# Kernel optimization log

Measured on AMD Instinct MI355X. Metric: run time of the kernel, lower is better.

Reference implementation:

```python
import jax, jax.numpy as jnp
import numpy as np
jax.config.update("jax_enable_x64", True)

PAD_ID = -1
NUM_DISCRETE = 128  # args.n_discrete_size

def _lexsort3(v):
    # torch code: stable argsort by x, then y, then z -> final key order z (primary), y, x.
    # numpy/jax lexsort: last key is primary, and it is stable.
    idx = jnp.lexsort((v[:, 0], v[:, 1], v[:, 2]))
    return v[idx], idx

def setup_inputs() -> dict:
    key = jax.random.key(0)
    k1, k2 = jax.random.split(key)
    B, NV, NF = 32, 32768, 65536
    vertices = jax.random.normal(k1, (B, NV, 3), dtype=jnp.float32)
    faces = jax.random.randint(k2, (B, NF, 3), 0, NV, dtype=jnp.int64)
    n_pad = NF // 10
    faces = faces.at[:, NF - n_pad:, :].set(PAD_ID)
    return {"vertices": vertices, "faces": faces}

def reference(vertices, faces):
    B, NV, _ = vertices.shape
    # normalize_vertices reduces over dim 0 (which is the BATCH dim here) - faithful to source
    mn = vertices.min(axis=0)
    mx = vertices.max(axis=0)
    center = (mn + mx) * 0.5
    longest = (mx - mn).max()
    v = (vertices - center) / longest
    # batched lexicographic sort of vertices
    sorted_v, sort_idx = jax.vmap(_lexsort3)(v)
    # inverse permutation (inv[sort_idx] = arange  <=>  argsort of a permutation)
    inv = jnp.argsort(sort_idx, axis=1)  # (B, NV)
    # torch indexes inverse_mapping[faces] with pad -1 wrapping to NV-1
    wrapped = jnp.mod(faces, NV)
    reindexed = jax.vmap(lambda m, f: m[f])(inv, wrapped)  # (B, NF, 3)
    sorted_faces, _ = jax.vmap(_lexsort3)(reindexed)
    # face mask: all three vertex ids != pad
    face_mask = jnp.all(faces != PAD_ID, axis=-1)  # (B, NF)
    face_np = jnp.where(face_mask[..., None], faces, 0)
    # gather vertex coords per face: (B, NF, 3verts, 3coords). The torch code
    # materializes a (b,nf,nv,3) repeat then gathers; we gather directly.
    face_coords = jax.vmap(lambda vv, ff: vv[ff])(sorted_v, face_np)
    # discretize into [-1, 1] -> [0, 127]
    t = (face_coords + 1.0) * 0.5 * NUM_DISCRETE - 0.5
    dq = jnp.clip(jnp.round(t).astype(jnp.int64), 0, NUM_DISCRETE - 1)
    codes = jnp.where(face_mask[..., None, None], dq, PAD_ID)
    input_ids = codes.reshape(B, -1)
    attention_mask = (input_ids != PAD_ID).astype(jnp.float32)
    ph = jnp.full((B, 1), PAD_ID, dtype=input_ids.dtype)
    input_ids = jnp.concatenate([ph, input_ids, ph], axis=1)
    attention_mask = jnp.concatenate([ph.astype(jnp.float32), attention_mask, ph.astype(jnp.float32)], axis=1)
    return input_ids, attention_mask, codes, dq, sorted_faces
```

## Files before the change

kernel.cpp:

```cpp
#include <hip/hip_runtime.h>
#include <stdint.h>

#define BATCH 32
#define NV 32768
#define NF 65536
#define PCOUNT (NV*3)


__device__ __forceinline__ unsigned fenc(float f){
  unsigned u = __float_as_uint(f);
  return (u & 0x80000000u) ? ~u : (u | 0x80000000u);
}
__device__ __forceinline__ float fdec(unsigned e){
  unsigned u = (e & 0x80000000u) ? (e & 0x7FFFFFFFu) : ~e;
  return __uint_as_float(u);
}

__global__ void kminmax(const float* __restrict__ vert, float* __restrict__ center,
                        unsigned* __restrict__ longestBits){
  int p = blockIdx.x*256 + threadIdx.x;
  float mn = 3.4e38f, mx = -3.4e38f;
  #pragma unroll
  for (int b = 0; b < BATCH; ++b) {
    float v = vert[(size_t)b*PCOUNT + p];
    mn = fminf(mn, v); mx = fmaxf(mx, v);
  }
  center[p] = __fadd_rn(mn, mx) * 0.5f;
  float r = __fsub_rn(mx, mn);
  for (int off = 32; off > 0; off >>= 1) r = fmaxf(r, __shfl_down(r, off, 64));
  if ((threadIdx.x & 63) == 0) atomicMax(longestBits, __float_as_uint(r));
}

__device__ __forceinline__ bool less4(uint4 a, uint4 b){
  if (a.x != b.x) return a.x < b.x;
  if (a.y != b.y) return a.y < b.y;
  if (a.z != b.z) return a.z < b.z;
  return a.w < b.w;
}
__device__ __forceinline__ bool less2(uint2 a, uint2 b){
  if (a.y != b.y) return a.y < b.y;
  return a.x < b.x;
}

#define VT 4096
#define FT 8192
#define SWV(i) ((i) ^ (((i) >> 3) & 7))
#define SWF(i) ((i) ^ (((i) >> 4) & 15))

__global__ __launch_bounds__(512) void klocalv(const float* __restrict__ vert,
                                               const float* __restrict__ center,
                                               const unsigned* __restrict__ longestBits,
                                               uint4* __restrict__ S){
  __shared__ uint4 sh[VT];
  int blockBase = blockIdx.x * VT;
  float L = __uint_as_float(*longestBits);
  float rl = __fdiv_rn(1.0f, L);
  for (int i = threadIdx.x; i < VT; i += 512){
    int id = blockBase + i;
    int vi = id & (NV-1);
    size_t vb = (size_t)(id >> 15)*PCOUNT + (size_t)vi*3;
    float nx = __fsub_rn(vert[vb+0], center[vi*3+0]);
    float ny = __fsub_rn(vert[vb+1], center[vi*3+1]);
    float nz = __fsub_rn(vert[vb+2], center[vi*3+2]);
    float x = __fmul_rn(nx, rl);
    float y = __fmul_rn(ny, rl);
    float z = __fmul_rn(nz, rl);
    uint4 s; s.x = fenc(z); s.y = fenc(y); s.z = fenc(x); s.w = (unsigned)vi;
    sh[SWV(i)] = s;
  }
  __syncthreads();
  int t = threadIdx.x;
  int k0 = t * 8;
  uint4 v[8];
  #pragma unroll
  for (int e = 0; e < 8; ++e) v[e] = sh[SWV(k0 + e)];
  #pragma unroll
  for (int k = 2; k <= 8; k <<= 1){
    #pragma unroll
    for (int j = k >> 1; j > 0; j >>= 1){
      #pragma unroll
      for (int i = 0; i < 8; ++i){
        int l = i ^ j;
        if (l > i){
          bool up = ((i & k) == 0);
          bool sw = up ? less4(v[l], v[i]) : less4(v[i], v[l]);
          if (sw){ uint4 tmp = v[i]; v[i] = v[l]; v[l] = tmp; }
        }
      }
    }
  }
  #pragma unroll
  for (int e = 0; e < 8; ++e) sh[SWV(k0 + e)] = v[e];
  __syncthreads();
  for (int w = 8; w < VT; w <<= 1){
    int base = k0 & ~(2*w - 1);
    int ko = k0 - base;
    int lo = ko - w; if (lo < 0) lo = 0;
    int hi = ko < w ? ko : w;
    while (lo < hi){
      int mid = (lo + hi) >> 1;
      if (less4(sh[SWV(base + mid)], sh[SWV(base + w + ko-1-mid)])) lo = mid + 1; else hi = mid;
    }
    int i = lo, j = ko - lo;
    uint4 m[8];
    #pragma unroll
    for (int e = 0; e < 8; ++e){
      bool takeA = (j >= w) || (i < w && less4(sh[SWV(base + i)], sh[SWV(base + w + j)]));
      m[e] = takeA ? sh[SWV(base + i)] : sh[SWV(base + w + j)];
      if (takeA) ++i; else ++j;
    }
    __syncthreads();
    #pragma unroll
    for (int e = 0; e < 8; ++e) sh[SWV(k0 + e)] = m[e];
    __syncthreads();
  }
  uint4* basep = S + (size_t)blockBase;
  for (int i = threadIdx.x; i < VT; i += 512) basep[i] = sh[SWV(i)];
}

__global__ __launch_bounds__(512) void klocalf(const int* __restrict__ faces,
                                               const int* __restrict__ inv,
                                               uint2* __restrict__ F){
  __shared__ uint2 sh[FT];
  int blockBase = blockIdx.x * FT;
  int b = blockBase >> 16;
  const int* invb = inv + (b << 15);
  for (int i = threadIdx.x; i < FT; i += 512){
    int id = blockBase + i;
    int f = id & (NF-1);
    size_t fb = (size_t)id*3;
    int f0 = faces[fb+0], f1 = faces[fb+1], f2 = faces[fb+2];
    unsigned r0 = (unsigned)invb[f0 & (NV-1)];
    unsigned r1 = (unsigned)invb[f1 & (NV-1)];
    unsigned r2 = (unsigned)invb[f2 & (NV-1)];
    uint2 r; r.x = (r0 << 15) | (unsigned)f; r.y = (r2 << 15) | r1;
    sh[SWF(i)] = r;
  }
  __syncthreads();
  int t = threadIdx.x;
  int k0 = t * 16;
  uint2 v[16];
  #pragma unroll
  for (int e = 0; e < 16; ++e) v[e] = sh[SWF(k0 + e)];
  #pragma unroll
  for (int k = 2; k <= 16; k <<= 1){
    #pragma unroll
    for (int j = k >> 1; j > 0; j >>= 1){
      #pragma unroll
      for (int i = 0; i < 16; ++i){
        int l = i ^ j;
        if (l > i){
          bool up = ((i & k) == 0);
          bool sw = up ? less2(v[l], v[i]) : less2(v[i], v[l]);
          if (sw){ uint2 tmp = v[i]; v[i] = v[l]; v[l] = tmp; }
        }
      }
    }
  }
  #pragma unroll
  for (int e = 0; e < 16; ++e) sh[SWF(k0 + e)] = v[e];
  __syncthreads();
  for (int w = 16; w < FT; w <<= 1){
    int base = k0 & ~(2*w - 1);
    int ko = k0 - base;
    int lo = ko - w; if (lo < 0) lo = 0;
    int hi = ko < w ? ko : w;
    while (lo < hi){
      int mid = (lo + hi) >> 1;
      if (less2(sh[SWF(base + mid)], sh[SWF(base + w + ko-1-mid)])) lo = mid + 1; else hi = mid;
    }
    int i = lo, j = ko - lo;
    uint2 m[16];
    #pragma unroll
    for (int e = 0; e < 16; ++e){
      bool takeA = (j >= w) || (i < w && less2(sh[SWF(base + i)], sh[SWF(base + w + j)]));
      m[e] = takeA ? sh[SWF(base + i)] : sh[SWF(base + w + j)];
      if (takeA) ++i; else ++j;
    }
    __syncthreads();
    #pragma unroll
    for (int e = 0; e < 16; ++e) sh[SWF(k0 + e)] = m[e];
    __syncthreads();
  }
  uint2* basep = F + (size_t)blockBase;
  for (int i = threadIdx.x; i < FT; i += 512) basep[i] = sh[SWF(i)];
}

__global__ __launch_bounds__(256) void kmergev(const uint4* __restrict__ src,
                                               uint4* __restrict__ dst, int L){
  __shared__ uint4 sh[2048];
  __shared__ int sAB[2];
  int gid = blockIdx.x;
  int b = gid >> 4, c = gid & 15;
  const uint4* base = src + ((size_t)b << 15);
  uint4* obase = dst + ((size_t)b << 15);
  int co = c * 2048;
  int pair = co / (2*L);
  int ko = co - pair*2*L;
  const uint4* A = base + (size_t)pair*2*L;
  const uint4* B = A + L;
  uint4* O = obase + (size_t)pair*2*L + ko;
  if (threadIdx.x < 2){
    int k = ko + (int)threadIdx.x * 2048;
    int lo = k - L; if (lo < 0) lo = 0;
    int hi = k < L ? k : L;
    while (lo < hi){
      int mid = (lo + hi) >> 1;
      if (less4(A[mid], B[k-1-mid])) lo = mid + 1; else hi = mid;
    }
    sAB[threadIdx.x] = lo;
  }
  __syncthreads();
  int aStart = sAB[0];
  int na = sAB[1] - aStart;
  int nb = 2048 - na;
  int bStart = ko - aStart;
  for (int i = threadIdx.x; i < 2048; i += 256)
    sh[i] = (i < na) ? A[aStart + i] : B[bStart + (i - na)];
  __syncthreads();
  int k0 = threadIdx.x * 8;
  int lo = k0 - nb; if (lo < 0) lo = 0;
  int hi = k0 < na ? k0 : na;
  while (lo < hi){
    int mid = (lo + hi) >> 1;
    if (less4(sh[mid], sh[na + k0-1-mid])) lo = mid + 1; else hi = mid;
  }
  int i = lo, j = k0 - lo;
  #pragma unroll
  for (int e = 0; e < 8; ++e){
    bool takeA = (j >= nb) || (i < na && less4(sh[i], sh[na + j]));
    uint4 v = takeA ? sh[i] : sh[na + j];
    if (takeA) ++i; else ++j;
    O[k0 + e] = v;
  }
}

__global__ __launch_bounds__(256) void kmergevQ(const uint4* __restrict__ src,
                                                int* __restrict__ inv,
                                                unsigned* __restrict__ Q){
  #pragma clang fp contract(off)
  __shared__ uint4 sh[2048];
  __shared__ int sAB[2];
  const int L = 16384;
  int gid = blockIdx.x;
  int b = gid >> 4, c = gid & 15;
  const uint4* A = src + ((size_t)b << 15);
  const uint4* B = A + L;
  int ko = c * 2048;
  if (threadIdx.x < 2){
    int k = ko + (int)threadIdx.x * 2048;
    int lo = k - L; if (lo < 0) lo = 0;
    int hi = k < L ? k : L;
    while (lo < hi){
      int mid = (lo + hi) >> 1;
      if (less4(A[mid], B[k-1-mid])) lo = mid + 1; else hi = mid;
    }
    sAB[threadIdx.x] = lo;
  }
  __syncthreads();
  int aStart = sAB[0];
  int na = sAB[1] - aStart;
  int nb = 2048 - na;
  int bStart = ko - aStart;
  for (int i = threadIdx.x; i < 2048; i += 256)
    sh[i] = (i < na) ? A[aStart + i] : B[bStart + (i - na)];
  __syncthreads();
  int k0 = threadIdx.x * 8;
  int lo = k0 - nb; if (lo < 0) lo = 0;
  int hi = k0 < na ? k0 : na;
  while (lo < hi){
    int mid = (lo + hi) >> 1;
    if (less4(sh[mid], sh[na + k0-1-mid])) lo = mid + 1; else hi = mid;
  }
  int i = lo, j = k0 - lo;
  #pragma unroll
  for (int e = 0; e < 8; ++e){
    bool takeA = (j >= nb) || (i < na && less4(sh[i], sh[na + j]));
    uint4 s = takeA ? sh[i] : sh[na + j];
    if (takeA) ++i; else ++j;
    int pos = ko + k0 + e;
    inv[(b<<15) + (int)s.w] = pos;
    float cco[3]; cco[0] = fdec(s.z); cco[1] = fdec(s.y); cco[2] = fdec(s.x);
    unsigned qw = 0;
    #pragma unroll
    for (int cc = 0; cc < 3; ++cc){
      float tt = ((cco[cc] + 1.0f) * 0.5f) * 128.0f - 0.5f;
      float rq = rintf(tt);
      int qi = (int)rq;
      qi = qi < 0 ? 0 : (qi > 127 ? 127 : qi);
      qw |= ((unsigned)qi) << (8*cc);
    }
    Q[(b<<15) + pos] = qw;
  }
}

__global__ __launch_bounds__(256) void kmergef(const uint2* __restrict__ src,
                                               uint2* __restrict__ dst, int L){
  __shared__ uint2 sh[2048];
  __shared__ int sAB[2];
  int gid = blockIdx.x;
  int b = gid >> 5, c = gid & 31;
  const uint2* base = src + ((size_t)b << 16);
  uint2* obase = dst + ((size_t)b << 16);
  int co = c * 2048;
  int pair = co / (2*L);
  int ko = co - pair*2*L;
  const uint2* A = base + (size_t)pair*2*L;
  const uint2* B = A + L;
  uint2* O = obase + (size_t)pair*2*L + ko;
  if (threadIdx.x < 2){
    int k = ko + (int)threadIdx.x * 2048;
    int lo = k - L; if (lo < 0) lo = 0;
    int hi = k < L ? k : L;
    while (lo < hi){
      int mid = (lo + hi) >> 1;
      if (less2(A[mid], B[k-1-mid])) lo = mid + 1; else hi = mid;
    }
    sAB[threadIdx.x] = lo;
  }
  __syncthreads();
  int aStart = sAB[0];
  int na = sAB[1] - aStart;
  int nb = 2048 - na;
  int bStart = ko - aStart;
  for (int i = threadIdx.x; i < 2048; i += 256)
    sh[i] = (i < na) ? A[aStart + i] : B[bStart + (i - na)];
  __syncthreads();
  int k0 = threadIdx.x * 8;
  int lo = k0 - nb; if (lo < 0) lo = 0;
  int hi = k0 < na ? k0 : na;
  while (lo < hi){
    int mid = (lo + hi) >> 1;
    if (less2(sh[mid], sh[na + k0-1-mid])) lo = mid + 1; else hi = mid;
  }
  int i = lo, j = k0 - lo;
  #pragma unroll
  for (int e = 0; e < 8; ++e){
    bool takeA = (j >= nb) || (i < na && less2(sh[i], sh[na + j]));
    uint2 v = takeA ? sh[i] : sh[na + j];
    if (takeA) ++i; else ++j;
    O[k0 + e] = v;
  }
}

__global__ __launch_bounds__(256) void kmergefOut(const uint2* __restrict__ src,
                                                  float* __restrict__ out){
  __shared__ __align__(16) float shf[6144];
  __shared__ int sAB[2];
  uint2* sh = (uint2*)shf;
  const int L = 32768;
  int gid = blockIdx.x;
  int b = gid >> 5, c = gid & 31;
  const uint2* A = src + ((size_t)b << 16);
  const uint2* B = A + L;
  int ko = c * 2048;
  if (threadIdx.x < 2){
    int k = ko + (int)threadIdx.x * 2048;
    int lo = k - L; if (lo < 0) lo = 0;
    int hi = k < L ? k : L;
    while (lo < hi){
      int mid = (lo + hi) >> 1;
      if (less2(A[mid], B[k-1-mid])) lo = mid + 1; else hi = mid;
    }
    sAB[threadIdx.x] = lo;
  }
  __syncthreads();
  int aStart = sAB[0];
  int na = sAB[1] - aStart;
  int nb = 2048 - na;
  int bStart = ko - aStart;
  for (int i = threadIdx.x; i < 2048; i += 256)
    sh[i] = (i < na) ? A[aStart + i] : B[bStart + (i - na)];
  __syncthreads();
  int k0 = threadIdx.x * 8;
  int lo = k0 - nb; if (lo < 0) lo = 0;
  int hi = k0 < na ? k0 : na;
  while (lo < hi){
    int mid = (lo + hi) >> 1;
    if (less2(sh[mid], sh[na + k0-1-mid])) lo = mid + 1; else hi = mid;
  }
  int i = lo, j = k0 - lo;
  uint2 v[8];
  #pragma unroll
  for (int e = 0; e < 8; ++e){
    bool takeA = (j >= nb) || (i < na && less2(sh[i], sh[na + j]));
    v[e] = takeA ? sh[i] : sh[na + j];
    if (takeA) ++i; else ++j;
  }
  __syncthreads();
  #pragma unroll
  for (int e = 0; e < 8; ++e){
    int o = (k0 + e) * 3;
    shf[o+0] = (float)(v[e].x >> 15);
    shf[o+1] = (float)(v[e].y & 0x7FFFu);
    shf[o+2] = (float)(v[e].y >> 15);
  }
  __syncthreads();
  size_t basef = 75497600 + ((size_t)b*65536 + (size_t)ko)*3;
  for (int q = threadIdx.x; q < 6144; q += 256) out[basef + q] = shf[q];
}

__global__ __launch_bounds__(256) void kfacesB(const int* __restrict__ faces,
                                               const unsigned* __restrict__ Q,
                                               float* __restrict__ out){
  __shared__ __align__(16) float shq[2304];
  __shared__ float shm[256];
  int p = blockIdx.x;
  int l = ((p & 7) << 10) | (p >> 3);
  int b = l >> 8, c = l & 255;
  int t = threadIdx.x;
  {
    size_t fb = ((size_t)(l*256 + t))*3;
    int f0 = faces[fb+0], f1 = faces[fb+1], f2 = faces[fb+2];
    bool mask = (f0 != -1) & (f1 != -1) & (f2 != -1);
    shm[t] = mask ? 1.0f : 0.0f;
    int fv[3] = {mask ? f0 : 0, mask ? f1 : 0, mask ? f2 : 0};
    #pragma unroll
    for (int k = 0; k < 3; ++k){
      unsigned qw = Q[(b<<15) + fv[k]];
      shq[t*9 + k*3 + 0] = (float)( qw        & 0xFFu);
      shq[t*9 + k*3 + 1] = (float)((qw >> 8 ) & 0xFFu);
      shq[t*9 + k*3 + 2] = (float)((qw >> 16) & 0xFFu);
    }
  }
  __syncthreads();
  float4* cp = (float4*)(out + 37748864 + (size_t)l*2304);
  float4* dp = (float4*)(out + 56623232 + (size_t)l*2304);
  for (int r = t; r < 576; r += 256){
    int e0 = r*4;
    float4 q = *(const float4*)&shq[e0];
    float m0 = shm[(unsigned)(e0  )/9u];
    float m1 = shm[(unsigned)(e0+1)/9u];
    float m2 = shm[(unsigned)(e0+2)/9u];
    float m3 = shm[(unsigned)(e0+3)/9u];
    float4 cv;
    cv.x = m0 != 0.0f ? q.x : -1.0f;
    cv.y = m1 != 0.0f ? q.y : -1.0f;
    cv.z = m2 != 0.0f ? q.z : -1.0f;
    cv.w = m3 != 0.0f ? q.w : -1.0f;
    cp[r] = cv;
    dp[r] = q;
  }
  size_t idsBase  = (size_t)b*589826 + 1 + (size_t)c*2304;
  size_t attnBase = 18874432 + idsBase;
  #pragma unroll
  for (int r = 0; r < 9; ++r){
    int idx = r*256 + t;
    float q = shq[idx];
    float m = shm[(unsigned)idx/9u];
    float cv = m != 0.0f ? q : -1.0f;
    out[idsBase + idx]  = cv;
    out[attnBase + idx] = m;
  }
  if (c == 0 && t == 0){
    out[(size_t)b*589826]                     = -1.0f;
    out[(size_t)b*589826 + 589825]            = -1.0f;
    out[18874432 + (size_t)b*589826]          = -1.0f;
    out[18874432 + (size_t)b*589826 + 589825] = -1.0f;
  }
}

extern "C" void kernel_launch(void* const* d_in, const int* in_sizes, int n_in,
                              void* d_out, int out_size, void* d_ws, size_t ws_size,
                              hipStream_t stream){
  const float* vert  = (const float*)d_in[0];
  const int*   faces = (const int*)d_in[1];
  float* out = (float*)d_out;

  uint4*    S           = (uint4*)d_ws;
  uint4*    S2          = (uint4*)((char*)d_ws + 16777216);
  uint2*    FKa         = (uint2*)((char*)d_ws + 16777216);
  unsigned* Q           = (unsigned*)((char*)d_ws + 16777216);
  uint2*    FKb         = (uint2*)d_ws;
  int*      inv         = (int*)((char*)d_ws + 33554432);
  float*    center      = (float*)((char*)d_ws + 37748736);
  unsigned* longestBits = (unsigned*)((char*)d_ws + 38141952);

  hipMemsetAsync(longestBits, 0, 4, stream);
  kminmax<<<PCOUNT/256, 256, 0, stream>>>(vert, center, longestBits);

  klocalv<<<BATCH*(NV/VT), 512, 0, stream>>>(vert, center, longestBits, S);
  kmergev<<<BATCH*16, 256, 0, stream>>>(S,  S2, 4096);
  kmergev<<<BATCH*16, 256, 0, stream>>>(S2, S,  8192);
  kmergevQ<<<BATCH*16, 256, 0, stream>>>(S, inv, Q);

  kfacesB<<<(BATCH*NF)/256, 256, 0, stream>>>(faces, Q, out);

  klocalf<<<BATCH*(NF/FT), 512, 0, stream>>>(faces, inv, FKa);
  kmergef<<<BATCH*32, 256, 0, stream>>>(FKa, FKb, 8192);
  kmergef<<<BATCH*32, 256, 0, stream>>>(FKb, FKa, 16384);
  kmergefOut<<<BATCH*32, 256, 0, stream>>>(FKa, out);
}
```

Before: 643.1 us.

## Fuse face code emission into local face sort kernel

Merges the per-face quantized-code and mask output kernel into the local face-sort kernel, so faces are read once and both the sort keys and the output codes come from the same load. Shared memory is reused as staging for code writes before the in-block sort. This removes one kernel launch and one full pass over the faces input, but it serializes 16 chunks per block with extra barriers and uses far fewer blocks for the output writes.

```diff
diff --git a/kernel.cpp b/kernel.cpp
--- a/kernel.cpp
+++ b/kernel.cpp
@@ -118,74 +118,6 @@
   for (int i = threadIdx.x; i < VT; i += 512) basep[i] = sh[SWV(i)];
 }
 
-__global__ __launch_bounds__(512) void klocalf(const int* __restrict__ faces,
-                                               const int* __restrict__ inv,
-                                               uint2* __restrict__ F){
-  __shared__ uint2 sh[FT];
-  int blockBase = blockIdx.x * FT;
-  int b = blockBase >> 16;
-  const int* invb = inv + (b << 15);
-  for (int i = threadIdx.x; i < FT; i += 512){
-    int id = blockBase + i;
-    int f = id & (NF-1);
-    size_t fb = (size_t)id*3;
-    int f0 = faces[fb+0], f1 = faces[fb+1], f2 = faces[fb+2];
-    unsigned r0 = (unsigned)invb[f0 & (NV-1)];
-    unsigned r1 = (unsigned)invb[f1 & (NV-1)];
-    unsigned r2 = (unsigned)invb[f2 & (NV-1)];
-    uint2 r; r.x = (r0 << 15) | (unsigned)f; r.y = (r2 << 15) | r1;
-    sh[SWF(i)] = r;
-  }
-  __syncthreads();
-  int t = threadIdx.x;
-  int k0 = t * 16;
-  uint2 v[16];
-  #pragma unroll
-  for (int e = 0; e < 16; ++e) v[e] = sh[SWF(k0 + e)];
-  #pragma unroll
-  for (int k = 2; k <= 16; k <<= 1){
-    #pragma unroll
-    for (int j = k >> 1; j > 0; j >>= 1){
-      #pragma unroll
-      for (int i = 0; i < 16; ++i){
-        int l = i ^ j;
-        if (l > i){
-          bool up = ((i & k) == 0);
-          bool sw = up ? less2(v[l], v[i]) : less2(v[i], v[l]);
-          if (sw){ uint2 tmp = v[i]; v[i] = v[l]; v[l] = tmp; }
-        }
-      }
-    }
-  }
-  #pragma unroll
-  for (int e = 0; e < 16; ++e) sh[SWF(k0 + e)] = v[e];
-  __syncthreads();
-  for (int w = 16; w < FT; w <<= 1){
-    int base = k0 & ~(2*w - 1);
-    int ko = k0 - base;
-    int lo = ko - w; if (lo < 0) lo = 0;
-    int hi = ko < w ? ko : w;
-    while (lo < hi){
-      int mid = (lo + hi) >> 1;
-      if (less2(sh[SWF(base + mid)], sh[SWF(base + w + ko-1-mid)])) lo = mid + 1; else hi = mid;
-    }
-    int i = lo, j = ko - lo;
-    uint2 m[16];
-    #pragma unroll
-    for (int e = 0; e < 16; ++e){
-      bool takeA = (j >= w) || (i < w && less2(sh[SWF(base + i)], sh[SWF(base + w + j)]));
-      m[e] = takeA ? sh[SWF(base + i)] : sh[SWF(base + w + j)];
-      if (takeA) ++i; else ++j;
-    }
-    __syncthreads();
-    #pragma unroll
-    for (int e = 0; e < 16; ++e) sh[SWF(k0 + e)] = m[e];
-    __syncthreads();
-  }
-  uint2* basep = F + (size_t)blockBase;
-  for (int i = threadIdx.x; i < FT; i += 512) basep[i] = sh[SWF(i)];
-}
-
 __global__ __launch_bounds__(256) void kmergev(const uint4* __restrict__ src,
                                                uint4* __restrict__ dst, int L){
   __shared__ uint4 sh[2048];
@@ -294,6 +226,128 @@
   }
 }
 
+__global__ __launch_bounds__(512) void klocalfB(const int* __restrict__ faces,
+                                                const int* __restrict__ inv,
+                                                const unsigned* __restrict__ Qt,
+                                                uint2* __restrict__ F,
+                                                float* __restrict__ out){
+  __shared__ __align__(16) uint2 sh[FT];
+  float* shq = (float*)sh;
+  float* shm = ((float*)sh) + 4608;
+  int blockBase = blockIdx.x * FT;
+  int b = blockBase >> 16;
+  const int* invb = inv + (b << 15);
+  const unsigned* Qb = Qt + (b << 15);
+  int t = threadIdx.x;
+  uint2 v[16];
+  #pragma unroll 16
+  for (int c = 0; c < 16; ++c){
+    int i = c*512 + t;
+    int id = blockBase + i;
+    int f = id & (NF-1);
+    size_t fb = (size_t)id*3;
+    int f0 = faces[fb+0], f1 = faces[fb+1], f2 = faces[fb+2];
+    bool mask = (f0 != -1) & (f1 != -1) & (f2 != -1);
+    unsigned r0 = (unsigned)invb[f0 & (NV-1)];
+    unsigned r1 = (unsigned)invb[f1 & (NV-1)];
+    unsigned r2 = (unsigned)invb[f2 & (NV-1)];
+    v[c].x = (r0 << 15) | (unsigned)f;
+    v[c].y = (r2 << 15) | r1;
+    unsigned qw0 = Qb[mask ? f0 : 0];
+    unsigned qw1 = Qb[mask ? f1 : 0];
+    unsigned qw2 = Qb[mask ? f2 : 0];
+    shm[t] = mask ? 1.0f : 0.0f;
+    shq[t*9+0] = (float)( qw0        & 255u);
+    shq[t*9+1] = (float)((qw0 >> 8 ) & 255u);
+    shq[t*9+2] = (float)((qw0 >> 16) & 255u);
+    shq[t*9+3] = (float)( qw1        & 255u);
+    shq[t*9+4] = (float)((qw1 >> 8 ) & 255u);
+    shq[t*9+5] = (float)((qw1 >> 16) & 255u);
+    shq[t*9+6] = (float)( qw2        & 255u);
+    shq[t*9+7] = (float)((qw2 >> 8 ) & 255u);
+    shq[t*9+8] = (float)((qw2 >> 16) & 255u);
+    __syncthreads();
+    float4* cp = (float4*)(out + 37748864 + ((size_t)blockBase + c*512)*9);
+    float4* dp = (float4*)(out + 56623232 + ((size_t)blockBase + c*512)*9);
+    for (int r = t; r < 1152; r += 512){
+      int e0 = r*4;
+      float4 q = *(const float4*)&shq[e0];
+      float m0 = shm[(unsigned)(e0  )/9u];
+      float m1 = shm[(unsigned)(e0+1)/9u];
+      float m2 = shm[(unsigned)(e0+2)/9u];
+      float m3 = shm[(unsigned)(e0+3)/9u];
+      float4 cv;
+      cv.x = m0 != 0.0f ? q.x : -1.0f;
+      cv.y = m1 != 0.0f ? q.y : -1.0f;
+      cv.z = m2 != 0.0f ? q.z : -1.0f;
+      cv.w = m3 != 0.0f ? q.w : -1.0f;
+      cp[r] = cv;
+      dp[r] = q;
+    }
+    size_t fi = (size_t)(blockBase & (NF-1)) + (size_t)c*512;
+    size_t idsBase  = (size_t)b*589826 + 1 + fi*9;
+    size_t attnBase = 18874432 + idsBase;
+    #pragma unroll
+    for (int r = 0; r < 9; ++r){
+      int idx = r*512 + t;
+      float q = shq[idx];
+      float m = shm[(unsigned)idx/9u];
+      out[idsBase + idx]  = m != 0.0f ? q : -1.0f;
+      out[attnBase + idx] = m;
+    }
+    __syncthreads();
+  }
+  if ((blockBase & (NF-1)) == 0 && t == 0){
+    out[(size_t)b*589826]                     = -1.0f;
+    out[(size_t)b*589826 + 589825]            = -1.0f;
+    out[18874432 + (size_t)b*589826]          = -1.0f;
+    out[18874432 + (size_t)b*589826 + 589825] = -1.0f;
+  }
+  #pragma unroll
+  for (int k = 2; k <= 16; k <<= 1){
+    #pragma unroll
+    for (int j = k >> 1; j > 0; j >>= 1){
+      #pragma unroll
+      for (int i = 0; i < 16; ++i){
+        int l = i ^ j;
+        if (l > i){
+          bool up = ((i & k) == 0);
+          bool sw = up ? less2(v[l], v[i]) : less2(v[i], v[l]);
+          if (sw){ uint2 tmp = v[i]; v[i] = v[l]; v[l] = tmp; }
+        }
+      }
+    }
+  }
+  int k0 = t * 16;
+  #pragma unroll
+  for (int e = 0; e < 16; ++e) sh[SWF(k0 + e)] = v[e];
+  __syncthreads();
+  for (int w = 16; w < FT; w <<= 1){
+    int base = k0 & ~(2*w - 1);
+    int ko = k0 - base;
+    int lo = ko - w; if (lo < 0) lo = 0;
+    int hi = ko < w ? ko : w;
+    while (lo < hi){
+      int mid = (lo + hi) >> 1;
+      if (less2(sh[SWF(base + mid)], sh[SWF(base + w + ko-1-mid)])) lo = mid + 1; else hi = mid;
+    }
+    int i = lo, j = ko - lo;
+    uint2 m[16];
+    #pragma unroll
+    for (int e = 0; e < 16; ++e){
+      bool takeA = (j >= w) || (i < w && less2(sh[SWF(base + i)], sh[SWF(base + w + j)]));
+      m[e] = takeA ? sh[SWF(base + i)] : sh[SWF(base + w + j)];
+      if (takeA) ++i; else ++j;
+    }
+    __syncthreads();
+    #pragma unroll
+    for (int e = 0; e < 16; ++e) sh[SWF(k0 + e)] = m[e];
+    __syncthreads();
+  }
+  uint2* basep = F + (size_t)blockBase;
+  for (int i = threadIdx.x; i < FT; i += 512) basep[i] = sh[SWF(i)];
+}
+
 __global__ __launch_bounds__(256) void kmergef(const uint2* __restrict__ src,
                                                uint2* __restrict__ dst, int L){
   __shared__ uint2 sh[2048];
@@ -400,66 +454,6 @@
   for (int q = threadIdx.x; q < 6144; q += 256) out[basef + q] = shf[q];
 }
 
-__global__ __launch_bounds__(256) void kfacesB(const int* __restrict__ faces,
-                                               const unsigned* __restrict__ Q,
-                                               float* __restrict__ out){
-  __shared__ __align__(16) float shq[2304];
-  __shared__ float shm[256];
-  int p = blockIdx.x;
-  int l = ((p & 7) << 10) | (p >> 3);
-  int b = l >> 8, c = l & 255;
-  int t = threadIdx.x;
-  {
-    size_t fb = ((size_t)(l*256 + t))*3;
-    int f0 = faces[fb+0], f1 = faces[fb+1], f2 = faces[fb+2];
-    bool mask = (f0 != -1) & (f1 != -1) & (f2 != -1);
-    shm[t] = mask ? 1.0f : 0.0f;
-    int fv[3] = {mask ? f0 : 0, mask ? f1 : 0, mask ? f2 : 0};
-    #pragma unroll
-    for (int k = 0; k < 3; ++k){
-      unsigned qw = Q[(b<<15) + fv[k]];
-      shq[t*9 + k*3 + 0] = (float)( qw        & 0xFFu);
-      shq[t*9 + k*3 + 1] = (float)((qw >> 8 ) & 0xFFu);
-      shq[t*9 + k*3 + 2] = (float)((qw >> 16) & 0xFFu);
-    }
-  }
-  __syncthreads();
-  float4* cp = (float4*)(out + 37748864 + (size_t)l*2304);
-  float4* dp = (float4*)(out + 56623232 + (size_t)l*2304);
-  for (int r = t; r < 576; r += 256){
-    int e0 = r*4;
-    float4 q = *(const float4*)&shq[e0];
-    float m0 = shm[(unsigned)(e0  )/9u];
-    float m1 = shm[(unsigned)(e0+1)/9u];
-    float m2 = shm[(unsigned)(e0+2)/9u];
-    float m3 = shm[(unsigned)(e0+3)/9u];
-    float4 cv;
-    cv.x = m0 != 0.0f ? q.x : -1.0f;
-    cv.y = m1 != 0.0f ? q.y : -1.0f;
-    cv.z = m2 != 0.0f ? q.z : -1.0f;
-    cv.w = m3 != 0.0f ? q.w : -1.0f;
-    cp[r] = cv;
-    dp[r] = q;
-  }
-  size_t idsBase  = (size_t)b*589826 + 1 + (size_t)c*2304;
-  size_t attnBase = 18874432 + idsBase;
-  #pragma unroll
-  for (int r = 0; r < 9; ++r){
-    int idx = r*256 + t;
-    float q = shq[idx];
-    float m = shm[(unsigned)idx/9u];
-    float cv = m != 0.0f ? q : -1.0f;
-    out[idsBase + idx]  = cv;
-    out[attnBase + idx] = m;
-  }
-  if (c == 0 && t == 0){
-    out[(size_t)b*589826]                     = -1.0f;
-    out[(size_t)b*589826 + 589825]            = -1.0f;
-    out[18874432 + (size_t)b*589826]          = -1.0f;
-    out[18874432 + (size_t)b*589826 + 589825] = -1.0f;
-  }
-}
-
 extern "C" void kernel_launch(void* const* d_in, const int* in_sizes, int n_in,
                               void* d_out, int out_size, void* d_ws, size_t ws_size,
                               hipStream_t stream){
@@ -484,10 +478,9 @@
   kmergev<<<BATCH*16, 256, 0, stream>>>(S2, S,  8192);
   kmergevQ<<<BATCH*16, 256, 0, stream>>>(S, inv, Q);
 
-  kfacesB<<<(BATCH*NF)/256, 256, 0, stream>>>(faces, Q, out);
-
-  klocalf<<<BATCH*(NF/FT), 512, 0, stream>>>(faces, inv, FKa);
-  kmergef<<<BATCH*32, 256, 0, stream>>>(FKa, FKb, 8192);
-  kmergef<<<BATCH*32, 256, 0, stream>>>(FKb, FKa, 16384);
-  kmergefOut<<<BATCH*32, 256, 0, stream>>>(FKa, out);
-}
+  klocalfB<<<BATCH*(NF/FT), 512, 0, stream>>>(faces, inv, Q, FKb, out);
+
+  kmergef<<<BATCH*32, 256, 0, stream>>>(FKb, FKa, 8192);
+  kmergef<<<BATCH*32, 256, 0, stream>>>(FKa, FKb, 16384);
+  kmergefOut<<<BATCH*32, 256, 0, stream>>>(FKb, out);
+}
```

Result: slower. 694.1 us (+7.9%).
